# Kernel optimization log

Measured on AMD Instinct MI355X. Metric: run time of the kernel, lower is better.

## Reference

```python
import jax, jax.numpy as jnp
import numpy as np

DT = 0.1
LN_EPS = 1e-5
B, T, D_IN, H, N_APP = 128, 2048, 16, 256, 10


def layer_norm(x, g, b):
    mu = jnp.mean(x, axis=-1, keepdims=True)
    var = jnp.mean(jnp.square(x - mu), axis=-1, keepdims=True)
    return (x - mu) * jax.lax.rsqrt(var + LN_EPS) * g + b


def setup_inputs() -> dict:
    key = jax.random.key(0)
    ks = jax.random.split(key, 4)
    x = jax.random.normal(ks[0], (B, T, D_IN), dtype=jnp.float32)
    W_in = jax.random.normal(ks[1], (H, D_IN), dtype=jnp.float32) * (1.0 / np.sqrt(D_IN))
    b_in = jnp.zeros((H,), dtype=jnp.float32)
    tau_param = jnp.ones((H,), dtype=jnp.float32)
    # xavier_uniform for (H, H)
    limit = np.sqrt(6.0 / (H + H))
    W_rec = jax.random.uniform(ks[2], (H, H), dtype=jnp.float32, minval=-limit, maxval=limit)
    g_intra = jnp.ones((H,), dtype=jnp.float32)
    b_intra = jnp.zeros((H,), dtype=jnp.float32)
    g_norm = jnp.ones((H,), dtype=jnp.float32)
    b_norm = jnp.zeros((H,), dtype=jnp.float32)
    W_head = jax.random.normal(ks[3], (H, N_APP), dtype=jnp.float32) * (1.0 / np.sqrt(H))
    b_head = jnp.zeros((N_APP,), dtype=jnp.float32)
    return dict(x=x, W_in=W_in, b_in=b_in, tau_param=tau_param, W_rec=W_rec,
                g_intra=g_intra, b_intra=b_intra, g_norm=g_norm, b_norm=b_norm,
                W_head=W_head, b_head=b_head)


def reference(x, W_in, b_in, tau_param, W_rec, g_intra, b_intra, g_norm, b_norm, W_head, b_head):
    # x: (B, T, D_IN)
    tau = jax.nn.softplus(tau_param)  # (H,), fixed
    # Precompute input projection for all timesteps: (B, T, H)
    inp_proj = jnp.einsum('bti,hi->bth', x, W_in) + b_in
    xs = jnp.swapaxes(inp_proj, 0, 1)  # (T, B, H) for scan

    def step(h, u_t):
        rec = h @ W_rec                       # (B, H)
        f_t = jnp.tanh(layer_norm(u_t + rec, g_intra, b_intra))
        dh = (-h / tau + f_t) * DT
        h_new = jnp.clip(h + dh, -10.0, 10.0)
        return h_new, None

    h0 = jnp.zeros((x.shape[0], W_rec.shape[0]), dtype=x.dtype)
    h, _ = jax.lax.scan(step, h0, xs)
    h = layer_norm(h, g_norm, b_norm)
    return h @ W_head + b_head  # (B, N_APP)
```

## Files before the change

### kernel.cpp

```cpp
#include <hip/hip_runtime.h>


#define BB     128
#define TT     2048
#define DIN    16
#define HH     256
#define NAPP   10
#define NT     256
#define DT_STEP 0.1f
#define LN_EPS_C 1e-5f

typedef _Float16 half2_t __attribute__((ext_vector_type(2)));

template<int CTRL>
__device__ __forceinline__ float dpp_mov0(float x) {
    return __builtin_bit_cast(float,
        __builtin_amdgcn_update_dpp(0, __builtin_bit_cast(int, x), CTRL, 0xF, 0xF, true));
}

__device__ __forceinline__ void wave_reduce2(float& s1, float& s2) {
    s1 += dpp_mov0<0x111>(s1); s2 += dpp_mov0<0x111>(s2);
    s1 += dpp_mov0<0x112>(s1); s2 += dpp_mov0<0x112>(s2);
    s1 += dpp_mov0<0x114>(s1); s2 += dpp_mov0<0x114>(s2);
    s1 += dpp_mov0<0x118>(s1); s2 += dpp_mov0<0x118>(s2);
    s1 += dpp_mov0<0x142>(s1); s2 += dpp_mov0<0x142>(s2);
    s1 += dpp_mov0<0x143>(s1); s2 += dpp_mov0<0x143>(s2);
}

__device__ __forceinline__ half2_t as_h2(int v) { return __builtin_bit_cast(half2_t, v); }
__device__ __forceinline__ float rl63(float v) {
    return __builtin_bit_cast(float,
        __builtin_amdgcn_readlane(__builtin_bit_cast(int, v), 63));
}
__device__ __forceinline__ float softplus_f(float v) {
    return (v > 20.f) ? v : log1pf(__expf(v));
}

__global__ __launch_bounds__(NT, 1)
void liquid_scan_kernel(const float* __restrict__ x,
                        const float* __restrict__ W_in,
                        const float* __restrict__ b_in,
                        const float* __restrict__ tau_param,
                        const float* __restrict__ W_rec,
                        const float* __restrict__ g_intra,
                        const float* __restrict__ b_intra,
                        const float* __restrict__ g_norm,
                        const float* __restrict__ b_norm,
                        const float* __restrict__ W_head,
                        const float* __restrict__ b_head,
                        float* __restrict__ out)
{
    const int tid  = threadIdx.x;
    const int b    = blockIdx.x;
    const int lane = tid & 63;
    const int kq   = tid >> 6;
    const int j0   = lane * 4;

    __shared__ __align__(16) float x_lds[TT * DIN];
    __shared__ __align__(16) float part[2][4][HH];

    {
        const float4* xg = (const float4*)(x + (size_t)b * TT * DIN);
        float4* xl = (float4*)x_lds;
        #pragma unroll 4
        for (int i = tid; i < TT * DIN / 4; i += NT) xl[i] = xg[i];
    }

    half2_t w2[4][32];
    #pragma unroll
    for (int p = 0; p < 32; ++p) {
        const float* r0 = W_rec + (size_t)(64 * kq + 2 * p) * HH + j0;
        const float* r1 = r0 + HH;
        #pragma unroll
        for (int c = 0; c < 4; ++c) {
            half2_t t2; t2.x = (_Float16)r0[c]; t2.y = (_Float16)r1[c];
            w2[c][p] = t2;
        }
    }

    float win[4][4];
    #pragma unroll
    for (int c = 0; c < 4; ++c) {
        #pragma unroll
        for (int r = 0; r < 4; ++r)
            win[c][r] = W_in[(size_t)(j0 + c) * DIN + 4 * kq + r];
    }

    float bi_[4], gi_[4], bbi_[4], itau_[4], gn_[4], bn_[4];
    {
        const float4 v0 = *(const float4*)(b_in      + j0);
        const float4 v1 = *(const float4*)(g_intra   + j0);
        const float4 v2 = *(const float4*)(b_intra   + j0);
        const float4 v3 = *(const float4*)(tau_param + j0);
        const float4 v4 = *(const float4*)(g_norm    + j0);
        const float4 v5 = *(const float4*)(b_norm    + j0);
        bi_[0] = v0.x; bi_[1] = v0.y; bi_[2] = v0.z; bi_[3] = v0.w;
        gi_[0] = v1.x; gi_[1] = v1.y; gi_[2] = v1.z; gi_[3] = v1.w;
        bbi_[0] = v2.x; bbi_[1] = v2.y; bbi_[2] = v2.z; bbi_[3] = v2.w;
        itau_[0] = 1.f / softplus_f(v3.x); itau_[1] = 1.f / softplus_f(v3.y);
        itau_[2] = 1.f / softplus_f(v3.z); itau_[3] = 1.f / softplus_f(v3.w);
        gn_[0] = v4.x; gn_[1] = v4.y; gn_[2] = v4.z; gn_[3] = v4.w;
        bn_[0] = v5.x; bn_[1] = v5.y; bn_[2] = v5.z; bn_[3] = v5.w;
    }

    float hj[4] = {0.f, 0.f, 0.f, 0.f};
    int pkX = 0, pkY = 0;
    const int rlbase = 16 * kq;
    const int o1 = (kq + 1) & 3, o2 = (kq + 2) & 3, o3 = (kq + 3) & 3;

    __syncthreads();

    #pragma unroll 1
    for (int t = 0; t < TT; ++t) {
        const float4 xs = *(const float4*)&x_lds[t * DIN + 4 * kq];

        float a0 = 0.f, a1 = 0.f, a2 = 0.f, a3 = 0.f;
        #pragma unroll
        for (int p = 0; p < 32; ++p) {
            const int r = __builtin_amdgcn_readlane((p & 1) ? pkY : pkX,
                                                    rlbase + (p >> 1));
            a0 = __builtin_amdgcn_fdot2(as_h2(r), w2[0][p], a0, false);
            a1 = __builtin_amdgcn_fdot2(as_h2(r), w2[1][p], a1, false);
            a2 = __builtin_amdgcn_fdot2(as_h2(r), w2[2][p], a2, false);
            a3 = __builtin_amdgcn_fdot2(as_h2(r), w2[3][p], a3, false);
        }
        a0 = fmaf(xs.x, win[0][0], a0); a0 = fmaf(xs.y, win[0][1], a0);
        a0 = fmaf(xs.z, win[0][2], a0); a0 = fmaf(xs.w, win[0][3], a0);
        a1 = fmaf(xs.x, win[1][0], a1); a1 = fmaf(xs.y, win[1][1], a1);
        a1 = fmaf(xs.z, win[1][2], a1); a1 = fmaf(xs.w, win[1][3], a1);
        a2 = fmaf(xs.x, win[2][0], a2); a2 = fmaf(xs.y, win[2][1], a2);
        a2 = fmaf(xs.z, win[2][2], a2); a2 = fmaf(xs.w, win[2][3], a2);
        a3 = fmaf(xs.x, win[3][0], a3); a3 = fmaf(xs.y, win[3][1], a3);
        a3 = fmaf(xs.z, win[3][2], a3); a3 = fmaf(xs.w, win[3][3], a3);

        ((float4*)part[t & 1][kq])[lane] = make_float4(a0, a1, a2, a3);
        __syncthreads();

        const float4 p1 = ((const float4*)part[t & 1][o1])[lane];
        const float4 p2 = ((const float4*)part[t & 1][o2])[lane];
        const float4 p3 = ((const float4*)part[t & 1][o3])[lane];
        float u[4];
        u[0] = (a0 + p1.x) + (p2.x + p3.x) + bi_[0];
        u[1] = (a1 + p1.y) + (p2.y + p3.y) + bi_[1];
        u[2] = (a2 + p1.z) + (p2.z + p3.z) + bi_[2];
        u[3] = (a3 + p1.w) + (p2.w + p3.w) + bi_[3];

        float s1 = (u[0] + u[1]) + (u[2] + u[3]);
        float s2 = (u[0] * u[0] + u[1] * u[1]) + (u[2] * u[2] + u[3] * u[3]);
        wave_reduce2(s1, s2);
        const float S1 = rl63(s1);
        const float S2 = rl63(s2);
        const float mu  = S1 * (1.f / HH);
        const float var = S2 * (1.f / HH) - mu * mu;
        const float rs  = __builtin_amdgcn_rsqf(var + LN_EPS_C);
        #pragma unroll
        for (int c = 0; c < 4; ++c) {
            const float xn = (u[c] - mu) * rs * gi_[c] + bbi_[c];
            const float e = __expf(2.f * xn);
            const float f = 1.f - 2.f * __builtin_amdgcn_rcpf(e + 1.f);
            float v = hj[c] + (f - hj[c] * itau_[c]) * DT_STEP;
            v = fminf(10.f, fmaxf(-10.f, v));
            hj[c] = v;
        }
        pkX = __builtin_bit_cast(int, __builtin_amdgcn_cvt_pkrtz(hj[0], hj[1]));
        pkY = __builtin_bit_cast(int, __builtin_amdgcn_cvt_pkrtz(hj[2], hj[3]));
    }

    if (kq == 0) {
        float s1 = (hj[0] + hj[1]) + (hj[2] + hj[3]);
        float s2 = (hj[0] * hj[0] + hj[1] * hj[1]) + (hj[2] * hj[2] + hj[3] * hj[3]);
        wave_reduce2(s1, s2);
        const float S1 = rl63(s1);
        const float S2 = rl63(s2);
        const float mu  = S1 * (1.f / HH);
        const float var = S2 * (1.f / HH) - mu * mu;
        const float rs  = rsqrtf(var + LN_EPS_C);
        float4 ho;
        ho.x = (hj[0] - mu) * rs * gn_[0] + bn_[0];
        ho.y = (hj[1] - mu) * rs * gn_[1] + bn_[1];
        ho.z = (hj[2] - mu) * rs * gn_[2] + bn_[2];
        ho.w = (hj[3] - mu) * rs * gn_[3] + bn_[3];
        ((float4*)part[0][0])[lane] = ho;
    }
    __syncthreads();
    if (tid < NAPP) {
        float o = b_head[tid];
        for (int jj = 0; jj < HH; ++jj)
            o = fmaf(part[0][0][jj], W_head[jj * NAPP + tid], o);
        out[(size_t)b * NAPP + tid] = o;
    }
}

extern "C" void kernel_launch(void* const* d_in, const int* in_sizes, int n_in,
                              void* d_out, int out_size, void* d_ws, size_t ws_size,
                              hipStream_t stream) {
    const float* x       = (const float*)d_in[0];
    const float* W_in    = (const float*)d_in[1];
    const float* b_in    = (const float*)d_in[2];
    const float* tau     = (const float*)d_in[3];
    const float* W_rec   = (const float*)d_in[4];
    const float* g_intra = (const float*)d_in[5];
    const float* b_intra = (const float*)d_in[6];
    const float* g_norm  = (const float*)d_in[7];
    const float* b_norm  = (const float*)d_in[8];
    const float* W_head  = (const float*)d_in[9];
    const float* b_head  = (const float*)d_in[10];
    float* out = (float*)d_out;

    hipLaunchKernelGGL(liquid_scan_kernel, dim3(BB), dim3(NT), 0, stream,
                       x, W_in, b_in, tau, W_rec, g_intra, b_intra,
                       g_norm, b_norm, W_head, b_head, out);
}
```

Measured before the change: 1.756 ms.

## Replace per-step block barrier with LDS flag spin-wait and simplify tanh update math

```diff
diff --git a/kernel.cpp b/kernel.cpp
--- a/kernel.cpp
+++ b/kernel.cpp
@@ -9,6 +9,7 @@
 #define NT     256
 #define DT_STEP 0.1f
 #define LN_EPS_C 1e-5f
+#define LOG2E2  2.8853900817779268f
 
 typedef _Float16 half2_t __attribute__((ext_vector_type(2)));
 
@@ -34,6 +35,11 @@
 }
 __device__ __forceinline__ float softplus_f(float v) {
     return (v > 20.f) ? v : log1pf(__expf(v));
+}
+__device__ __forceinline__ float exp2_fast(float v) {
+    float r;
+    asm("v_exp_f32 %0, %1" : "=v"(r) : "v"(v));
+    return r;
 }
 
 __global__ __launch_bounds__(NT, 1)
@@ -56,8 +62,9 @@
     const int kq   = tid >> 6;
     const int j0   = lane * 4;
 
-    __shared__ __align__(16) float x_lds[TT * DIN];
-    __shared__ __align__(16) float part[2][4][HH];
+    __shared__ __align__(16) float    x_lds[TT * DIN];
+    __shared__ __align__(16) float    part[2][4][HH];
+    __shared__ __align__(16) unsigned flags[4];
 
     {
         const float4* xg = (const float4*)(x + (size_t)b * TT * DIN);
@@ -65,6 +72,7 @@
         #pragma unroll 4
         for (int i = tid; i < TT * DIN / 4; i += NT) xl[i] = xg[i];
     }
+    if (tid < 4) flags[tid] = 0u;
 
     half2_t w2[4][32];
     #pragma unroll
@@ -86,7 +94,7 @@
             win[c][r] = W_in[(size_t)(j0 + c) * DIN + 4 * kq + r];
     }
 
-    float bi_[4], gi_[4], bbi_[4], itau_[4], gn_[4], bn_[4];
+    float bi_[4], gi2_[4], bbi2_[4], dec_[4], gn_[4], bn_[4];
     {
         const float4 v0 = *(const float4*)(b_in      + j0);
         const float4 v1 = *(const float4*)(g_intra   + j0);
@@ -95,10 +103,14 @@
         const float4 v4 = *(const float4*)(g_norm    + j0);
         const float4 v5 = *(const float4*)(b_norm    + j0);
         bi_[0] = v0.x; bi_[1] = v0.y; bi_[2] = v0.z; bi_[3] = v0.w;
-        gi_[0] = v1.x; gi_[1] = v1.y; gi_[2] = v1.z; gi_[3] = v1.w;
-        bbi_[0] = v2.x; bbi_[1] = v2.y; bbi_[2] = v2.z; bbi_[3] = v2.w;
-        itau_[0] = 1.f / softplus_f(v3.x); itau_[1] = 1.f / softplus_f(v3.y);
-        itau_[2] = 1.f / softplus_f(v3.z); itau_[3] = 1.f / softplus_f(v3.w);
+        gi2_[0] = v1.x * LOG2E2; gi2_[1] = v1.y * LOG2E2;
+        gi2_[2] = v1.z * LOG2E2; gi2_[3] = v1.w * LOG2E2;
+        bbi2_[0] = v2.x * LOG2E2; bbi2_[1] = v2.y * LOG2E2;
+        bbi2_[2] = v2.z * LOG2E2; bbi2_[3] = v2.w * LOG2E2;
+        dec_[0] = 1.f - DT_STEP / softplus_f(v3.x);
+        dec_[1] = 1.f - DT_STEP / softplus_f(v3.y);
+        dec_[2] = 1.f - DT_STEP / softplus_f(v3.z);
+        dec_[3] = 1.f - DT_STEP / softplus_f(v3.w);
         gn_[0] = v4.x; gn_[1] = v4.y; gn_[2] = v4.z; gn_[3] = v4.w;
         bn_[0] = v5.x; bn_[1] = v5.y; bn_[2] = v5.z; bn_[3] = v5.w;
     }
@@ -107,6 +119,7 @@
     int pkX = 0, pkY = 0;
     const int rlbase = 16 * kq;
     const int o1 = (kq + 1) & 3, o2 = (kq + 2) & 3, o3 = (kq + 3) & 3;
+    volatile unsigned* vfl = (volatile unsigned*)flags;
 
     __syncthreads();
 
@@ -133,8 +146,15 @@
         a3 = fmaf(xs.x, win[3][0], a3); a3 = fmaf(xs.y, win[3][1], a3);
         a3 = fmaf(xs.z, win[3][2], a3); a3 = fmaf(xs.w, win[3][3], a3);
 
+        const unsigned tgt = (unsigned)(t + 1);
         ((float4*)part[t & 1][kq])[lane] = make_float4(a0, a1, a2, a3);
-        __syncthreads();
+        asm volatile("s_waitcnt lgkmcnt(0)" ::: "memory");
+        if (lane == 0) vfl[kq] = tgt;
+        unsigned f1, f2, f3;
+        do {
+            f1 = vfl[o1]; f2 = vfl[o2]; f3 = vfl[o3];
+        } while (f1 < tgt || f2 < tgt || f3 < tgt);
+        asm volatile("" ::: "memory");
 
         const float4 p1 = ((const float4*)part[t & 1][o1])[lane];
         const float4 p2 = ((const float4*)part[t & 1][o2])[lane];
@@ -155,10 +175,11 @@
         const float rs  = __builtin_amdgcn_rsqf(var + LN_EPS_C);
         #pragma unroll
         for (int c = 0; c < 4; ++c) {
-            const float xn = (u[c] - mu) * rs * gi_[c] + bbi_[c];
-            const float e = __expf(2.f * xn);
-            const float f = 1.f - 2.f * __builtin_amdgcn_rcpf(e + 1.f);
-            float v = hj[c] + (f - hj[c] * itau_[c]) * DT_STEP;
+            const float xn2 = fmaf((u[c] - mu) * rs, gi2_[c], bbi2_[c]);
+            const float e   = exp2_fast(xn2);
+            const float r   = __builtin_amdgcn_rcpf(e + 1.f);
+            const float fdt = fmaf(-2.f * DT_STEP, r, DT_STEP);
+            float v = fmaf(hj[c], dec_[c], fdt);
             v = fminf(10.f, fmaxf(-10.f, v));
             hj[c] = v;
         }
```

Result: slower. 1.906 ms (+8.5%).
